# Performance work log

Hardware: AMD Instinct MI355X
Metric: run time of the kernel (lower is better)

## Reference

```python
import jax, jax.numpy as jnp
import numpy as np

D_MODEL = 1024
D_FF = 2048        # SwiGLU hidden (first linear outputs 2*D_FF)
NUM_EXPERTS = 8
TOP_K = 2
BATCH, SEQ = 2, 2048


def setup_inputs() -> dict:
    key = jax.random.key(0)
    ks = jax.random.split(key, 5)
    s = 0.02
    x = jax.random.normal(ks[0], (BATCH, SEQ, D_MODEL), jnp.float32)
    Wr = jax.random.normal(ks[1], (D_MODEL, NUM_EXPERTS), jnp.float32) * s
    temp = jnp.ones((1,), jnp.float32)  # router_temp parameter
    W1 = jax.random.normal(ks[2], (NUM_EXPERTS, D_MODEL, 2 * D_FF), jnp.float32) * s
    b1 = jnp.zeros((NUM_EXPERTS, 2 * D_FF), jnp.float32)
    W2 = jax.random.normal(ks[3], (NUM_EXPERTS, D_FF, D_MODEL), jnp.float32) * s
    b2 = jnp.zeros((NUM_EXPERTS, D_MODEL), jnp.float32)
    return {"x": x, "Wr": Wr, "temp": temp, "W1": W1, "b1": b1, "W2": W2, "b2": b2}


def reference(x, Wr, temp, W1, b1, W2, b2):
    # Eval-mode forward: no router noise, dropout is identity.
    B, S, D = x.shape
    xf = x.reshape(-1, D)                       # [T, D], T = B*S
    logits = (xf @ Wr) / temp                   # [T, E]
    topw, topi = jax.lax.top_k(logits, TOP_K)   # [T, K]
    topw = jax.nn.softmax(topw, axis=-1)        # renormalized top-k weights
    out = jnp.zeros_like(xf)
    for e in range(NUM_EXPERTS):                # small fixed expert count
        h = xf @ W1[e] + b1[e]                  # [T, 2F]
        a, g = jnp.split(h, 2, axis=-1)         # SwiGLU: a * silu(g)
        y = (a * jax.nn.silu(g)) @ W2[e] + b2[e]  # [T, D]
        # combine weight for expert e (0 if not routed to e)
        we = jnp.sum(jnp.where(topi == e, topw, 0.0), axis=-1, keepdims=True)
        out = out + y * we
    return out.reshape(B, S, D)
```

## Files before the change

### kernel.cpp

```cpp
#include <hip/hip_runtime.h>
#include <hip/hip_bf16.h>
#include <math.h>


#define T_TOK  4096
#define DMODEL 1024
#define NEXP   8
#define FF     2048
#define FF2    4096

typedef __bf16 bf16_t;
typedef bf16_t bf16x8 __attribute__((ext_vector_type(8)));
typedef float  f32x4  __attribute__((ext_vector_type(4)));

__device__ __forceinline__ void gload_lds16(const void* g, void* l) {
  __builtin_amdgcn_global_load_lds((const __attribute__((address_space(1))) void*)g,
                                   (__attribute__((address_space(3))) void*)l, 16, 0, 0);
}

__global__ __launch_bounds__(256) void moe_router(
    const float* __restrict__ x, const float* __restrict__ Wr,
    const float* __restrict__ temp,
    bf16_t* __restrict__ xb,
    int* __restrict__ cnt, int* __restrict__ tok_list, float* __restrict__ w_list,
    int* __restrict__ slot)
{
  __shared__ float sWr[DMODEL * NEXP];
  for (int i = threadIdx.x; i < DMODEL * NEXP; i += 256) sWr[i] = Wr[i];
  __syncthreads();

  int wave = threadIdx.x >> 6, lane = threadIdx.x & 63;
  int t = blockIdx.x * 4 + wave;
  const float* xr = x + (size_t)t * DMODEL;

  f32x4 acc0 = {0.f, 0.f, 0.f, 0.f}, acc1 = {0.f, 0.f, 0.f, 0.f};
  #pragma unroll
  for (int i = 0; i < 16; ++i) {
    int d = lane + 64 * i;
    float v = xr[d];
    xb[(size_t)t * DMODEL + d] = (bf16_t)v;
    const f32x4* wr = (const f32x4*)&sWr[d * NEXP];
    acc0 += v * wr[0];
    acc1 += v * wr[1];
  }
  #pragma unroll
  for (int off = 32; off; off >>= 1) {
    #pragma unroll
    for (int q = 0; q < 4; ++q) {
      acc0[q] += __shfl_down(acc0[q], off, 64);
      acc1[q] += __shfl_down(acc1[q], off, 64);
    }
  }
  if (lane == 0) {
    float invt = 1.f / temp[0];
    float lg[NEXP] = {acc0[0], acc0[1], acc0[2], acc0[3],
                      acc1[0], acc1[1], acc1[2], acc1[3]};
    int bi = 0, si = 0;
    float best = -3.4e38f, sec = -3.4e38f;
    #pragma unroll
    for (int e = 0; e < NEXP; ++e) {
      float l = lg[e] * invt;
      if (l > best)     { sec = best; si = bi; best = l; bi = e; }
      else if (l > sec) { sec = l; si = e; }
    }
    float ex = expf(sec - best);
    float wb  = 1.f / (1.f + ex);
    float wsc = ex  / (1.f + ex);
    int p0 = atomicAdd(&cnt[bi], 1);
    tok_list[bi * T_TOK + p0] = t; w_list[bi * T_TOK + p0] = wb;
    int p1 = atomicAdd(&cnt[si], 1);
    tok_list[si * T_TOK + p1] = t; w_list[si * T_TOK + p1] = wsc;
    slot[2 * t]     = bi * T_TOK + p0;
    slot[2 * t + 1] = si * T_TOK + p1;
  }
}

__global__ void moe_prefix(const int* __restrict__ cnt, int* __restrict__ offs) {
  if (threadIdx.x == 0) {
    int s = 0;
    for (int e = 0; e < NEXP; ++e) { offs[e] = s; s += cnt[e]; }
    offs[NEXP] = s;
  }
}

__global__ __launch_bounds__(256) void tcast_fast(
    const float* __restrict__ in, bf16_t* __restrict__ outp, int R, int C)
{
  __shared__ float tile[64][65];
  const float* inp = in + (size_t)blockIdx.z * R * C;
  bf16_t* op = outp + (size_t)blockIdx.z * R * C;
  int c0 = blockIdx.x * 64, r0 = blockIdx.y * 64;
  int tid = threadIdx.x;
  int lr = tid >> 4;
  int lc4 = (tid & 15) * 4;
  #pragma unroll
  for (int p = 0; p < 4; ++p) {
    int r = p * 16 + lr;
    const float4 v = *(const float4*)&inp[(size_t)(r0 + r) * C + c0 + lc4];
    tile[r][lc4 + 0] = v.x; tile[r][lc4 + 1] = v.y;
    tile[r][lc4 + 2] = v.z; tile[r][lc4 + 3] = v.w;
  }
  __syncthreads();
  int rr8 = (tid & 7) * 8;
  #pragma unroll
  for (int it = 0; it < 2; ++it) {
    int cc = (tid >> 3) + it * 32;
    bf16x8 o;
    #pragma unroll
    for (int j = 0; j < 8; ++j) o[j] = (bf16_t)tile[rr8 + j][cc];
    *(bf16x8*)&op[(size_t)(c0 + cc) * R + r0 + rr8] = o;
  }
}

__global__ __launch_bounds__(256) void moe_gemm1(
    const bf16_t* __restrict__ xb, const bf16_t* __restrict__ W1t,
    const float* __restrict__ b1, const int* __restrict__ cnt,
    const int* __restrict__ offs, const int* __restrict__ tok_list,
    const float* __restrict__ w_list, bf16_t* __restrict__ U,
    int e_base, long estride)
{
  int e = e_base + blockIdx.z;
  int count = cnt[e];
  int m0 = blockIdx.y * 128;
  if (m0 >= count) return;
  int nt = blockIdx.x;
  const bf16_t* W1e = W1t + (size_t)blockIdx.z * estride;

  __shared__ bf16_t As[128 * 64];
  __shared__ bf16_t Bs[128 * 64];
  __shared__ int   stok[128];
  __shared__ float sw[128];
  int tid = threadIdx.x;
  if (tid < 128) {
    int m = m0 + tid;
    stok[tid] = (m < count) ? tok_list[e * T_TOK + m] : 0;
    sw[tid]   = (m < count) ? w_list[e * T_TOK + m] : 0.f;
  }
  __syncthreads();

  int wave = tid >> 6, lane = tid & 63;
  int quad = lane >> 4, l16 = lane & 15;
  int rsub = lane >> 3;
  int swz  = (lane & 7) ^ rsub;

  size_t asrc[4]; const bf16_t* bsrc[4];
  bf16_t* aldst[4]; bf16_t* bldst[4];
  #pragma unroll
  for (int s = 0; s < 4; ++s) {
    int inst = wave * 4 + s;
    int row = inst * 8 + rsub;
    asrc[s] = (size_t)stok[row] * DMODEL + swz * 8;
    int grow = (row < 64) ? (nt * 64 + row) : (FF + nt * 64 + (row - 64));
    bsrc[s] = W1e + (size_t)grow * DMODEL + swz * 8;
    aldst[s] = As + inst * 512;
    bldst[s] = Bs + inst * 512;
  }

  f32x4 acc[2][8];
  #pragma unroll
  for (int i = 0; i < 2; ++i)
    #pragma unroll
    for (int j = 0; j < 8; ++j) acc[i][j] = (f32x4){0.f, 0.f, 0.f, 0.f};

  for (int k0 = 0; k0 < DMODEL; k0 += 64) {
    __syncthreads();
    #pragma unroll
    for (int s = 0; s < 4; ++s) {
      gload_lds16(xb + asrc[s] + k0, aldst[s]);
      gload_lds16(bsrc[s] + k0, bldst[s]);
    }
    __syncthreads();
    #pragma unroll
    for (int kh = 0; kh < 2; ++kh) {
      int so = ((kh * 4 + quad) ^ (l16 & 7)) * 8;
      bf16x8 a0 = *(const bf16x8*)&As[(wave * 32      + l16) * 64 + so];
      bf16x8 a1 = *(const bf16x8*)&As[(wave * 32 + 16 + l16) * 64 + so];
      #pragma unroll
      for (int j = 0; j < 8; ++j) {
        bf16x8 b = *(const bf16x8*)&Bs[(j * 16 + l16) * 64 + so];
        acc[0][j] = __builtin_amdgcn_mfma_f32_16x16x32_bf16(a0, b, acc[0][j], 0, 0, 0);
        acc[1][j] = __builtin_amdgcn_mfma_f32_16x16x32_bf16(a1, b, acc[1][j], 0, 0, 0);
      }
    }
  }

  int uoff = offs[e];
  const float* b1e = b1 + (size_t)e * FF2;
  #pragma unroll
  for (int j = 0; j < 4; ++j) {
    int f = nt * 64 + j * 16 + l16;
    float ba = b1e[f];
    float bg = b1e[FF + f];
    #pragma unroll
    for (int i = 0; i < 2; ++i) {
      f32x4 av = acc[i][j];
      f32x4 gv = acc[i][j + 4];
      #pragma unroll
      for (int r = 0; r < 4; ++r) {
        int m = wave * 32 + i * 16 + quad * 4 + r;
        if (m0 + m < count) {
          float aa = av[r] + ba;
          float gg = gv[r] + bg;
          float u = sw[m] * aa * gg / (1.f + __expf(-gg));
          U[(size_t)(uoff + m0 + m) * FF + f] = (bf16_t)u;
        }
      }
    }
  }
}

__global__ __launch_bounds__(256) void moe_gemm2(
    const bf16_t* __restrict__ U, const bf16_t* __restrict__ W2t,
    const int* __restrict__ cnt, const int* __restrict__ offs,
    float* __restrict__ Y,
    int e_base, long estride)
{
  int e = e_base + blockIdx.z;
  int count = cnt[e];
  int m0 = blockIdx.y * 128;
  if (m0 >= count) return;
  int n0 = blockIdx.x * 128;
  const bf16_t* W2e = W2t + (size_t)blockIdx.z * estride;

  __shared__ bf16_t As[128 * 64];
  __shared__ bf16_t Bs[128 * 64];
  int tid = threadIdx.x;
  int wave = tid >> 6, lane = tid & 63;
  int quad = lane >> 4, l16 = lane & 15;
  int rsub = lane >> 3;
  int swz  = (lane & 7) ^ rsub;
  int uoff = offs[e];

  const bf16_t* asrc[4]; const bf16_t* bsrc[4];
  bf16_t* aldst[4]; bf16_t* bldst[4];
  #pragma unroll
  for (int s = 0; s < 4; ++s) {
    int inst = wave * 4 + s;
    int row = inst * 8 + rsub;
    asrc[s] = U   + (size_t)(uoff + m0 + row) * FF + swz * 8;
    bsrc[s] = W2e + (size_t)(n0 + row)        * FF + swz * 8;
    aldst[s] = As + inst * 512;
    bldst[s] = Bs + inst * 512;
  }

  f32x4 acc[2][8];
  #pragma unroll
  for (int i = 0; i < 2; ++i)
    #pragma unroll
    for (int j = 0; j < 8; ++j) acc[i][j] = (f32x4){0.f, 0.f, 0.f, 0.f};

  for (int k0 = 0; k0 < FF; k0 += 64) {
    __syncthreads();
    #pragma unroll
    for (int s = 0; s < 4; ++s) {
      gload_lds16(asrc[s] + k0, aldst[s]);
      gload_lds16(bsrc[s] + k0, bldst[s]);
    }
    __syncthreads();
    #pragma unroll
    for (int kh = 0; kh < 2; ++kh) {
      int so = ((kh * 4 + quad) ^ (l16 & 7)) * 8;
      bf16x8 a0 = *(const bf16x8*)&As[(wave * 32      + l16) * 64 + so];
      bf16x8 a1 = *(const bf16x8*)&As[(wave * 32 + 16 + l16) * 64 + so];
      #pragma unroll
      for (int j = 0; j < 8; ++j) {
        bf16x8 b = *(const bf16x8*)&Bs[(j * 16 + l16) * 64 + so];
        acc[0][j] = __builtin_amdgcn_mfma_f32_16x16x32_bf16(a0, b, acc[0][j], 0, 0, 0);
        acc[1][j] = __builtin_amdgcn_mfma_f32_16x16x32_bf16(a1, b, acc[1][j], 0, 0, 0);
      }
    }
  }

  #pragma unroll
  for (int j = 0; j < 8; ++j) {
    int n = n0 + j * 16 + l16;
    #pragma unroll
    for (int i = 0; i < 2; ++i) {
      f32x4 av = acc[i][j];
      #pragma unroll
      for (int r = 0; r < 4; ++r) {
        int m = wave * 32 + i * 16 + quad * 4 + r;
        if (m0 + m < count)
          Y[(size_t)(uoff + m0 + m) * DMODEL + n] = av[r];
      }
    }
  }
}

__global__ __launch_bounds__(256) void moe_combine(
    const float* __restrict__ Y, const float* __restrict__ b2,
    const int* __restrict__ slot, const float* __restrict__ w_list,
    const int* __restrict__ offs, float* __restrict__ out)
{
  int t = blockIdx.x;
  int v0 = slot[2 * t], v1 = slot[2 * t + 1];
  int e0 = v0 >> 12, p0 = v0 & (T_TOK - 1);
  int e1 = v1 >> 12, p1 = v1 & (T_TOK - 1);
  int r0 = offs[e0] + p0, r1 = offs[e1] + p1;
  float w0 = w_list[v0], w1 = w_list[v1];
  int d = threadIdx.x * 4;
  f32x4 y0 = *(const f32x4*)&Y[(size_t)r0 * DMODEL + d];
  f32x4 y1 = *(const f32x4*)&Y[(size_t)r1 * DMODEL + d];
  f32x4 c0 = *(const f32x4*)&b2[(size_t)e0 * DMODEL + d];
  f32x4 c1 = *(const f32x4*)&b2[(size_t)e1 * DMODEL + d];
  *(f32x4*)&out[(size_t)t * DMODEL + d] = y0 + y1 + w0 * c0 + w1 * c1;
}

extern "C" void kernel_launch(void* const* d_in, const int* in_sizes, int n_in,
                              void* d_out, int out_size, void* d_ws, size_t ws_size,
                              hipStream_t stream)
{
  const float* x    = (const float*)d_in[0];
  const float* Wr   = (const float*)d_in[1];
  const float* temp = (const float*)d_in[2];
  const float* W1   = (const float*)d_in[3];
  const float* b1   = (const float*)d_in[4];
  const float* W2   = (const float*)d_in[5];
  const float* b2   = (const float*)d_in[6];
  float* out = (float*)d_out;

  char* ws = (char*)d_ws;
  size_t off = 0;
  auto alloc = [&](size_t b) { void* p = ws + off; off += (b + 255) & ~(size_t)255; return p; };
  bf16_t* xb  = (bf16_t*)alloc((size_t)T_TOK * DMODEL * 2);
  bf16_t* U   = (bf16_t*)alloc((size_t)(2 * T_TOK + 128) * FF * 2);
  float*  Y   = (float*)alloc((size_t)(2 * T_TOK) * DMODEL * 4);
  int*   cnt  = (int*)alloc(256);
  int*   offs = (int*)alloc(256);
  int*   tok  = (int*)alloc((size_t)NEXP * T_TOK * 4);
  float* wl   = (float*)alloc((size_t)NEXP * T_TOK * 4);
  int*   slot = (int*)alloc((size_t)2 * T_TOK * 4);
  size_t base = off;
  const size_t W1T_FULL = (size_t)NEXP * FF2 * DMODEL * 2;
  const size_t W2T_FULL = (size_t)NEXP * DMODEL * FF * 2;
  bool batched = (ws_size >= base + W1T_FULL + W2T_FULL);

  hipMemsetAsync(cnt, 0, NEXP * sizeof(int), stream);
  moe_router<<<dim3(T_TOK / 4), dim3(256), 0, stream>>>(x, Wr, temp, xb, cnt, tok, wl, slot);
  moe_prefix<<<dim3(1), dim3(64), 0, stream>>>(cnt, offs);

  if (batched) {
    bf16_t* W1t = (bf16_t*)alloc(W1T_FULL);
    bf16_t* W2t = (bf16_t*)alloc(W2T_FULL);
    tcast_fast<<<dim3(FF2 / 64, DMODEL / 64, NEXP), dim3(256), 0, stream>>>(W1, W1t, DMODEL, FF2);
    tcast_fast<<<dim3(DMODEL / 64, FF / 64, NEXP), dim3(256), 0, stream>>>(W2, W2t, FF, DMODEL);
    moe_gemm1<<<dim3(FF / 64, T_TOK / 128, NEXP), dim3(256), 0, stream>>>(
        xb, W1t, b1, cnt, offs, tok, wl, U, 0, (long)FF2 * DMODEL);
    moe_gemm2<<<dim3(DMODEL / 128, T_TOK / 128, NEXP), dim3(256), 0, stream>>>(
        U, W2t, cnt, offs, Y, 0, (long)DMODEL * FF);
  } else {
    bf16_t* W1t = (bf16_t*)alloc((size_t)FF2 * DMODEL * 2);
    bf16_t* W2t = (bf16_t*)alloc((size_t)DMODEL * FF * 2);
    for (int e = 0; e < NEXP; ++e) {
      tcast_fast<<<dim3(FF2 / 64, DMODEL / 64, 1), dim3(256), 0, stream>>>(
          W1 + (size_t)e * DMODEL * FF2, W1t, DMODEL, FF2);
      moe_gemm1<<<dim3(FF / 64, T_TOK / 128, 1), dim3(256), 0, stream>>>(
          xb, W1t, b1, cnt, offs, tok, wl, U, e, 0);
    }
    for (int e = 0; e < NEXP; ++e) {
      tcast_fast<<<dim3(DMODEL / 64, FF / 64, 1), dim3(256), 0, stream>>>(
          W2 + (size_t)e * FF * DMODEL, W2t, FF, DMODEL);
      moe_gemm2<<<dim3(DMODEL / 128, T_TOK / 128, 1), dim3(256), 0, stream>>>(
          U, W2t, cnt, offs, Y, e, 0);
    }
  }
  moe_combine<<<dim3(T_TOK), dim3(256), 0, stream>>>(Y, b2, slot, wl, offs, out);
}
```

Measured before the change: 538.9 us.

## Fuse weight transposes, drop prefix kernel, narrow gemm2 tiles, alias Y buffer

Merges the two weight transpose-cast launches into one kernel. Removes the separate prefix-sum launch by computing segment offsets from the expert counts inside gemm1, gemm2 and combine. Narrows the gemm2 N tile from 128 to 64 to put more blocks on the device, and reuses the W1t region for Y to save workspace. The aim is fewer launches and better occupancy in gemm2, at the cost of more A-tile reloads in gemm2. Aliasing Y onto W1t relies on gemm1 finishing before gemm2 writes Y.

```diff
diff --git a/kernel.cpp b/kernel.cpp
--- a/kernel.cpp
+++ b/kernel.cpp
@@ -16,6 +16,13 @@
 __device__ __forceinline__ void gload_lds16(const void* g, void* l) {
   __builtin_amdgcn_global_load_lds((const __attribute__((address_space(1))) void*)g,
                                    (__attribute__((address_space(3))) void*)l, 16, 0, 0);
+}
+
+__device__ __forceinline__ int seg_off(const int* __restrict__ cnt, int e) {
+  int s = 0;
+  #pragma unroll
+  for (int i = 0; i < NEXP; ++i) s += (i < e) ? cnt[i] : 0;
+  return s;
 }
 
 __global__ __launch_bounds__(256) void moe_router(
@@ -75,21 +82,10 @@
   }
 }
 
-__global__ void moe_prefix(const int* __restrict__ cnt, int* __restrict__ offs) {
-  if (threadIdx.x == 0) {
-    int s = 0;
-    for (int e = 0; e < NEXP; ++e) { offs[e] = s; s += cnt[e]; }
-    offs[NEXP] = s;
-  }
-}
-
-__global__ __launch_bounds__(256) void tcast_fast(
-    const float* __restrict__ in, bf16_t* __restrict__ outp, int R, int C)
-{
-  __shared__ float tile[64][65];
-  const float* inp = in + (size_t)blockIdx.z * R * C;
-  bf16_t* op = outp + (size_t)blockIdx.z * R * C;
-  int c0 = blockIdx.x * 64, r0 = blockIdx.y * 64;
+__device__ __forceinline__ void tcast_tile(
+    const float* __restrict__ inp, bf16_t* __restrict__ op,
+    int R, int C, int r0, int c0, float (*tile)[65])
+{
   int tid = threadIdx.x;
   int lr = tid >> 4;
   int lc4 = (tid & 15) * 4;
@@ -112,10 +108,37 @@
   }
 }
 
+__global__ __launch_bounds__(256) void tcast_fused(
+    const float* __restrict__ W1, bf16_t* __restrict__ W1t,
+    const float* __restrict__ W2, bf16_t* __restrict__ W2t)
+{
+  __shared__ float tile[64][65];
+  int z = blockIdx.z;
+  if (z < NEXP) {
+    const float* inp = W1 + (size_t)z * DMODEL * FF2;
+    bf16_t* op = W1t + (size_t)z * DMODEL * FF2;
+    tcast_tile(inp, op, DMODEL, FF2, blockIdx.y * 64, blockIdx.x * 64, tile);
+  } else {
+    int idx = blockIdx.y * 64 + blockIdx.x;
+    int e = (z - NEXP) * 2 + (idx >> 9);
+    int i = idx & 511;
+    const float* inp = W2 + (size_t)e * FF * DMODEL;
+    bf16_t* op = W2t + (size_t)e * FF * DMODEL;
+    tcast_tile(inp, op, FF, DMODEL, (i >> 4) * 64, (i & 15) * 64, tile);
+  }
+}
+
+__global__ __launch_bounds__(256) void tcast_fast(
+    const float* __restrict__ in, bf16_t* __restrict__ outp, int R, int C)
+{
+  __shared__ float tile[64][65];
+  tcast_tile(in, outp, R, C, blockIdx.y * 64, blockIdx.x * 64, tile);
+}
+
 __global__ __launch_bounds__(256) void moe_gemm1(
     const bf16_t* __restrict__ xb, const bf16_t* __restrict__ W1t,
     const float* __restrict__ b1, const int* __restrict__ cnt,
-    const int* __restrict__ offs, const int* __restrict__ tok_list,
+    const int* __restrict__ tok_list,
     const float* __restrict__ w_list, bf16_t* __restrict__ U,
     int e_base, long estride)
 {
@@ -184,7 +207,7 @@
     }
   }
 
-  int uoff = offs[e];
+  int uoff = seg_off(cnt, e);
   const float* b1e = b1 + (size_t)e * FF2;
   #pragma unroll
   for (int j = 0; j < 4; ++j) {
@@ -211,51 +234,54 @@
 
 __global__ __launch_bounds__(256) void moe_gemm2(
     const bf16_t* __restrict__ U, const bf16_t* __restrict__ W2t,
-    const int* __restrict__ cnt, const int* __restrict__ offs,
-    float* __restrict__ Y,
+    const int* __restrict__ cnt, float* __restrict__ Y,
     int e_base, long estride)
 {
   int e = e_base + blockIdx.z;
   int count = cnt[e];
   int m0 = blockIdx.y * 128;
   if (m0 >= count) return;
-  int n0 = blockIdx.x * 128;
+  int n0 = blockIdx.x * 64;
   const bf16_t* W2e = W2t + (size_t)blockIdx.z * estride;
+  int uoff = seg_off(cnt, e);
 
   __shared__ bf16_t As[128 * 64];
-  __shared__ bf16_t Bs[128 * 64];
+  __shared__ bf16_t Bs[64 * 64];
   int tid = threadIdx.x;
   int wave = tid >> 6, lane = tid & 63;
   int quad = lane >> 4, l16 = lane & 15;
   int rsub = lane >> 3;
   int swz  = (lane & 7) ^ rsub;
-  int uoff = offs[e];
-
-  const bf16_t* asrc[4]; const bf16_t* bsrc[4];
-  bf16_t* aldst[4]; bf16_t* bldst[4];
+
+  const bf16_t* asrc[4]; bf16_t* aldst[4];
   #pragma unroll
   for (int s = 0; s < 4; ++s) {
     int inst = wave * 4 + s;
     int row = inst * 8 + rsub;
-    asrc[s] = U   + (size_t)(uoff + m0 + row) * FF + swz * 8;
-    bsrc[s] = W2e + (size_t)(n0 + row)        * FF + swz * 8;
+    asrc[s] = U + (size_t)(uoff + m0 + row) * FF + swz * 8;
     aldst[s] = As + inst * 512;
+  }
+  const bf16_t* bsrc[2]; bf16_t* bldst[2];
+  #pragma unroll
+  for (int s = 0; s < 2; ++s) {
+    int inst = wave * 2 + s;
+    int row = inst * 8 + rsub;
+    bsrc[s] = W2e + (size_t)(n0 + row) * FF + swz * 8;
     bldst[s] = Bs + inst * 512;
   }
 
-  f32x4 acc[2][8];
+  f32x4 acc[2][4];
   #pragma unroll
   for (int i = 0; i < 2; ++i)
     #pragma unroll
-    for (int j = 0; j < 8; ++j) acc[i][j] = (f32x4){0.f, 0.f, 0.f, 0.f};
+    for (int j = 0; j < 4; ++j) acc[i][j] = (f32x4){0.f, 0.f, 0.f, 0.f};
 
   for (int k0 = 0; k0 < FF; k0 += 64) {
     __syncthreads();
     #pragma unroll
-    for (int s = 0; s < 4; ++s) {
-      gload_lds16(asrc[s] + k0, aldst[s]);
-      gload_lds16(bsrc[s] + k0, bldst[s]);
-    }
+    for (int s = 0; s < 4; ++s) gload_lds16(asrc[s] + k0, aldst[s]);
+    #pragma unroll
+    for (int s = 0; s < 2; ++s) gload_lds16(bsrc[s] + k0, bldst[s]);
     __syncthreads();
     #pragma unroll
     for (int kh = 0; kh < 2; ++kh) {
@@ -263,7 +289,7 @@
       bf16x8 a0 = *(const bf16x8*)&As[(wave * 32      + l16) * 64 + so];
       bf16x8 a1 = *(const bf16x8*)&As[(wave * 32 + 16 + l16) * 64 + so];
       #pragma unroll
-      for (int j = 0; j < 8; ++j) {
+      for (int j = 0; j < 4; ++j) {
         bf16x8 b = *(const bf16x8*)&Bs[(j * 16 + l16) * 64 + so];
         acc[0][j] = __builtin_amdgcn_mfma_f32_16x16x32_bf16(a0, b, acc[0][j], 0, 0, 0);
         acc[1][j] = __builtin_amdgcn_mfma_f32_16x16x32_bf16(a1, b, acc[1][j], 0, 0, 0);
@@ -272,7 +298,7 @@
   }
 
   #pragma unroll
-  for (int j = 0; j < 8; ++j) {
+  for (int j = 0; j < 4; ++j) {
     int n = n0 + j * 16 + l16;
     #pragma unroll
     for (int i = 0; i < 2; ++i) {
@@ -290,13 +316,21 @@
 __global__ __launch_bounds__(256) void moe_combine(
     const float* __restrict__ Y, const float* __restrict__ b2,
     const int* __restrict__ slot, const float* __restrict__ w_list,
-    const int* __restrict__ offs, float* __restrict__ out)
-{
+    const int* __restrict__ cnt, float* __restrict__ out)
+{
+  __shared__ int pre[NEXP];
+  if (threadIdx.x < NEXP) {
+    int s = 0;
+    #pragma unroll
+    for (int i = 0; i < NEXP; ++i) s += (i < (int)threadIdx.x) ? cnt[i] : 0;
+    pre[threadIdx.x] = s;
+  }
+  __syncthreads();
   int t = blockIdx.x;
   int v0 = slot[2 * t], v1 = slot[2 * t + 1];
   int e0 = v0 >> 12, p0 = v0 & (T_TOK - 1);
   int e1 = v1 >> 12, p1 = v1 & (T_TOK - 1);
-  int r0 = offs[e0] + p0, r1 = offs[e1] + p1;
+  int r0 = pre[e0] + p0, r1 = pre[e1] + p1;
   float w0 = w_list[v0], w1 = w_list[v1];
   int d = threadIdx.x * 4;
   f32x4 y0 = *(const f32x4*)&Y[(size_t)r0 * DMODEL + d];
@@ -324,9 +358,7 @@
   auto alloc = [&](size_t b) { void* p = ws + off; off += (b + 255) & ~(size_t)255; return p; };
   bf16_t* xb  = (bf16_t*)alloc((size_t)T_TOK * DMODEL * 2);
   bf16_t* U   = (bf16_t*)alloc((size_t)(2 * T_TOK + 128) * FF * 2);
-  float*  Y   = (float*)alloc((size_t)(2 * T_TOK) * DMODEL * 4);
   int*   cnt  = (int*)alloc(256);
-  int*   offs = (int*)alloc(256);
   int*   tok  = (int*)alloc((size_t)NEXP * T_TOK * 4);
   float* wl   = (float*)alloc((size_t)NEXP * T_TOK * 4);
   int*   slot = (int*)alloc((size_t)2 * T_TOK * 4);
@@ -337,32 +369,33 @@
 
   hipMemsetAsync(cnt, 0, NEXP * sizeof(int), stream);
   moe_router<<<dim3(T_TOK / 4), dim3(256), 0, stream>>>(x, Wr, temp, xb, cnt, tok, wl, slot);
-  moe_prefix<<<dim3(1), dim3(64), 0, stream>>>(cnt, offs);
 
   if (batched) {
     bf16_t* W1t = (bf16_t*)alloc(W1T_FULL);
     bf16_t* W2t = (bf16_t*)alloc(W2T_FULL);
-    tcast_fast<<<dim3(FF2 / 64, DMODEL / 64, NEXP), dim3(256), 0, stream>>>(W1, W1t, DMODEL, FF2);
-    tcast_fast<<<dim3(DMODEL / 64, FF / 64, NEXP), dim3(256), 0, stream>>>(W2, W2t, FF, DMODEL);
+    float*  Y   = (float*)W1t;
+    tcast_fused<<<dim3(64, 16, 12), dim3(256), 0, stream>>>(W1, W1t, W2, W2t);
     moe_gemm1<<<dim3(FF / 64, T_TOK / 128, NEXP), dim3(256), 0, stream>>>(
-        xb, W1t, b1, cnt, offs, tok, wl, U, 0, (long)FF2 * DMODEL);
-    moe_gemm2<<<dim3(DMODEL / 128, T_TOK / 128, NEXP), dim3(256), 0, stream>>>(
-        U, W2t, cnt, offs, Y, 0, (long)DMODEL * FF);
+        xb, W1t, b1, cnt, tok, wl, U, 0, (long)FF2 * DMODEL);
+    moe_gemm2<<<dim3(DMODEL / 64, T_TOK / 128, NEXP), dim3(256), 0, stream>>>(
+        U, W2t, cnt, Y, 0, (long)DMODEL * FF);
+    moe_combine<<<dim3(T_TOK), dim3(256), 0, stream>>>(Y, b2, slot, wl, cnt, out);
   } else {
+    float*  Y   = (float*)alloc((size_t)(2 * T_TOK) * DMODEL * 4);
     bf16_t* W1t = (bf16_t*)alloc((size_t)FF2 * DMODEL * 2);
     bf16_t* W2t = (bf16_t*)alloc((size_t)DMODEL * FF * 2);
     for (int e = 0; e < NEXP; ++e) {
       tcast_fast<<<dim3(FF2 / 64, DMODEL / 64, 1), dim3(256), 0, stream>>>(
           W1 + (size_t)e * DMODEL * FF2, W1t, DMODEL, FF2);
       moe_gemm1<<<dim3(FF / 64, T_TOK / 128, 1), dim3(256), 0, stream>>>(
-          xb, W1t, b1, cnt, offs, tok, wl, U, e, 0);
+          xb, W1t, b1, cnt, tok, wl, U, e, 0);
     }
     for (int e = 0; e < NEXP; ++e) {
       tcast_fast<<<dim3(DMODEL / 64, FF / 64, 1), dim3(256), 0, stream>>>(
           W2 + (size_t)e * FF * DMODEL, W2t, FF, DMODEL);
-      moe_gemm2<<<dim3(DMODEL / 128, T_TOK / 128, 1), dim3(256), 0, stream>>>(
-          U, W2t, cnt, offs, Y, e, 0);
-    }
-  }
-  moe_combine<<<dim3(T_TOK), dim3(256), 0, stream>>>(Y, b2, slot, wl, offs, out);
-}
+      moe_gemm2<<<dim3(DMODEL / 64, T_TOK / 128, 1), dim3(256), 0, stream>>>(
+          U, W2t, cnt, Y, e, 0);
+    }
+    moe_combine<<<dim3(T_TOK), dim3(256), 0, stream>>>(Y, b2, slot, wl, cnt, out);
+  }
+}
```

Measured after the change: 558.8 us. 3.7% more time.
